# Performance work log

Hardware: AMD Instinct MI355X
Metric: run time of the kernel (lower is better)

The kernel has to match this reference:

```python
import jax, jax.numpy as jnp
import numpy as np

N, D, H = 4096, 256, 8
NEG = -4294967295.0  # -2**32 + 1, as in masked_fill


def _layernorm(x, g, b, eps=1e-5):
    mu = jnp.mean(x, axis=-1, keepdims=True)
    var = jnp.var(x, axis=-1, keepdims=True)
    return (x - mu) * jax.lax.rsqrt(var + eps) * g + b


def setup_inputs() -> dict:
    key = jax.random.key(0)
    ks = jax.random.split(key, 12)
    s = 0.02
    return {
        "x": jax.random.normal(ks[0], (N, D), jnp.float32),
        "mask_idx": jax.random.randint(ks[1], (N,), 0, 2, jnp.int32),
        "spatial": jax.random.normal(ks[2], (N, N), jnp.float32),
        "edge": jax.random.normal(ks[3], (N, N), jnp.float32),
        "ln1_g": jnp.ones((D,), jnp.float32),
        "ln1_b": jnp.zeros((D,), jnp.float32),
        "Wq": jax.random.normal(ks[4], (H, D, D), jnp.float32) * s,
        "bq": jnp.zeros((H, D), jnp.float32),
        "Wk": jax.random.normal(ks[5], (H, D, D), jnp.float32) * s,
        "bk": jnp.zeros((H, D), jnp.float32),
        "Wv": jax.random.normal(ks[6], (H, D, D), jnp.float32) * s,
        "bv": jnp.zeros((H, D), jnp.float32),
        "Wo": jax.random.normal(ks[7], (D, H * D), jnp.float32) * s,
        "bo": jnp.zeros((D,), jnp.float32),
        "ln2_g": jnp.ones((D,), jnp.float32),
        "ln2_b": jnp.zeros((D,), jnp.float32),
        "Wff": jax.random.normal(ks[8], (D, D), jnp.float32) * s,
        "bff": jnp.zeros((D,), jnp.float32),
    }


def reference(x, mask_idx, spatial, edge, ln1_g, ln1_b, Wq, bq, Wk, bk, Wv, bv,
              Wo, bo, ln2_g, ln2_b, Wff, bff):
    x_ln = _layernorm(x, ln1_g, ln1_b)
    # per-head projections, torch Linear: y = x W^T + b ; q,k,v: [H, N, D]
    q = jnp.einsum('nd,hed->hne', x_ln, Wq) + bq[:, None, :]
    k = jnp.einsum('nd,hed->hne', x_ln, Wk) + bk[:, None, :]
    v = jnp.einsum('nd,hed->hne', x_ln, Wv) + bv[:, None, :]
    scale = 1.0 / jnp.sqrt(jnp.float32(D))  # dim_q ** 0.5
    a = jnp.einsum('hne,hme->hnm', q, k) * scale  # [H, N, N]
    a = a + spatial[None] + edge[None]
    mask0 = (mask_idx[:, None] * mask_idx[None, :]) == 0  # [N, N]
    a = jnp.where(mask0[None], jnp.float32(NEG), a)
    p = jax.nn.softmax(a, axis=-1)
    p = jnp.where(mask0[None], 0.0, p)
    heads = jnp.einsum('hnm,hme->hne', p, v)  # [H, N, D]
    cat = jnp.transpose(heads, (1, 0, 2)).reshape(N, H * D)
    x_out = cat @ Wo.T + bo + x
    x_attn = _layernorm(x_out, ln2_g, ln2_b) @ Wff.T + bff + x_out
    return x_attn
```

## Files before the change

### kernel.cpp

```cpp
#include <hip/hip_runtime.h>
#include <hip/hip_bf16.h>
#include <hip/hip_fp16.h>
#include <string.h>

typedef unsigned short u16;
typedef __attribute__((ext_vector_type(8))) short short8;
typedef __attribute__((ext_vector_type(4))) float floatx4;
typedef __attribute__((ext_vector_type(16))) float floatx16;

#define N_TOK 4096
#define D_DIM 256
#define H_HEAD 8

__device__ __forceinline__ u16 f2b(float f){
  __hip_bfloat16 h = __float2bfloat16(f);
  return *reinterpret_cast<u16*>(&h);
}
__device__ __forceinline__ float b2f(u16 u){
  union { unsigned u; float f; } c; c.u = ((unsigned)u) << 16; return c.f;
}
__device__ __forceinline__ float h2f(u16 u){
  __half h; *reinterpret_cast<u16*>(&h) = u; return __half2float(h);
}
__device__ __forceinline__ u16 f2h(float f){
  __half h = __float2half(f); return *reinterpret_cast<u16*>(&h);
}

__device__ __forceinline__ void glds16(const void* g, void* l){
  __builtin_amdgcn_global_load_lds(
      (const __attribute__((address_space(1))) unsigned int*)g,
      (__attribute__((address_space(3))) unsigned int*)l, 16, 0, 0);
}

__global__ void fused_prep(const float* __restrict__ Wq, const float* __restrict__ Wk,
                           const float* __restrict__ Wv, const float* __restrict__ Wo,
                           const float* __restrict__ Wff,
                           const float* __restrict__ bq, const float* __restrict__ bk,
                           const float* __restrict__ bv,
                           u16* __restrict__ wqkv, u16* __restrict__ wo_b,
                           u16* __restrict__ wff_b, float* __restrict__ bqkv){
  int bid = blockIdx.x;
  if (bid == 1056){
    int t = threadIdx.x;
    for (int j = 0; j < 24; ++j){
      int idx = t + j*256;
      float v;
      if (idx < 2048) v = bq[idx];
      else if (idx < 4096) v = bk[idx - 2048];
      else v = bv[idx - 4096];
      bqkv[idx] = v;
    }
    return;
  }
  const float* src; u16* dst; int base;
  if      (bid < 256) { src = Wq;  dst = wqkv;            base = bid; }
  else if (bid < 512) { src = Wk;  dst = wqkv + 524288;   base = bid - 256; }
  else if (bid < 768) { src = Wv;  dst = wqkv + 1048576;  base = bid - 512; }
  else if (bid < 1024){ src = Wo;  dst = wo_b;            base = bid - 768; }
  else                { src = Wff; dst = wff_b;           base = bid - 1024; }
  int i = (base*256 + threadIdx.x)*8;
  float4 a = *(const float4*)(src + i);
  float4 b = *(const float4*)(src + i + 4);
  u16 u[8] = {f2b(a.x),f2b(a.y),f2b(a.z),f2b(a.w),f2b(b.x),f2b(b.y),f2b(b.z),f2b(b.w)};
  *(short8*)(dst + i) = *(short8*)u;
}

__global__ void ln_kernel(const float* __restrict__ x, const float* __restrict__ g,
                          const float* __restrict__ b, u16* __restrict__ out){
  const int row = blockIdx.x;
  const int t = threadIdx.x;
  float v = x[(size_t)row*D_DIM + t];
  float s = v, ss = v*v;
  #pragma unroll
  for (int off = 32; off > 0; off >>= 1){
    s  += __shfl_down(s,  off);
    ss += __shfl_down(ss, off);
  }
  __shared__ float ls[4], lss[4];
  const int w = t >> 6, lane = t & 63;
  if (lane == 0){ ls[w] = s; lss[w] = ss; }
  __syncthreads();
  if (t == 0){
    float S  = ls[0]+ls[1]+ls[2]+ls[3];
    float SS = lss[0]+lss[1]+lss[2]+lss[3];
    float mu = S * (1.0f/D_DIM);
    float var = SS * (1.0f/D_DIM) - mu*mu;
    ls[0] = mu; lss[0] = rsqrtf(var + 1e-5f);
  }
  __syncthreads();
  float mu = ls[0], rs = lss[0];
  out[(size_t)row*D_DIM + t] = f2b((v - mu)*rs*g[t] + b[t]);
}

__global__ void make_biasW(const float* __restrict__ sp, const float* __restrict__ ed,
                           const int* __restrict__ mask, u16* __restrict__ out){
  __shared__ u16 bh[32][64];
  const int tg = blockIdx.x, q32 = blockIdx.y;
  const int t = threadIdx.x;
  const float L2E = 1.4426950408889634f;
  {
    int ql = t>>3, kc = (t&7)*8;
    size_t off = (size_t)(q32*32 + ql)*N_TOK + tg*64 + kc;
    float4 s0 = *(const float4*)(sp + off);
    float4 s1 = *(const float4*)(sp + off + 4);
    float4 e0 = *(const float4*)(ed + off);
    float4 e1 = *(const float4*)(ed + off + 4);
    int mr = mask[q32*32 + ql];
    int4 m0 = *(const int4*)(mask + tg*64 + kc);
    int4 m1 = *(const int4*)(mask + tg*64 + kc + 4);
    bh[ql][kc+0] = f2h((mr*m0.x)==0 ? -60000.f : (s0.x+e0.x)*L2E);
    bh[ql][kc+1] = f2h((mr*m0.y)==0 ? -60000.f : (s0.y+e0.y)*L2E);
    bh[ql][kc+2] = f2h((mr*m0.z)==0 ? -60000.f : (s0.z+e0.z)*L2E);
    bh[ql][kc+3] = f2h((mr*m0.w)==0 ? -60000.f : (s0.w+e0.w)*L2E);
    bh[ql][kc+4] = f2h((mr*m1.x)==0 ? -60000.f : (s1.x+e1.x)*L2E);
    bh[ql][kc+5] = f2h((mr*m1.y)==0 ? -60000.f : (s1.y+e1.y)*L2E);
    bh[ql][kc+6] = f2h((mr*m1.z)==0 ? -60000.f : (s1.z+e1.z)*L2E);
    bh[ql][kc+7] = f2h((mr*m1.w)==0 ? -60000.f : (s1.w+e1.w)*L2E);
  }
  __syncthreads();
  int lane2 = t>>2, j0 = (t&3)*8;
  u16 tmp[8];
  #pragma unroll
  for (int jj = 0; jj < 8; ++jj){
    int j = j0 + jj;
    int nb = j>>4, reg = j&15;
    int kvl = nb*32 + (reg&3) + 8*(reg>>2) + 4*(lane2>>5);
    tmp[jj] = bh[lane2&31][kvl];
  }
  u16* dst = out + (((size_t)q32*64 + tg)*64 + lane2)*32 + j0;
  *(short8*)dst = *(short8*)tmp;
}

__global__ void transpose_v(const u16* __restrict__ v, u16* __restrict__ vt){
  __shared__ u16 t[64][72];
  const int h = blockIdx.z;
  const int n0 = blockIdx.x*64, e0 = blockIdx.y*64;
  const int tid = threadIdx.x;
  const int r = tid >> 2;
  const int c = (tid & 3)*16;
  const u16* src = v + ((size_t)h*N_TOK + n0 + r)*D_DIM + e0 + c;
  short8 a = *(const short8*)src;
  short8 b = *(const short8*)(src + 8);
  #pragma unroll
  for (int i = 0; i < 8; ++i){ t[r][c+i] = ((u16*)&a)[i]; t[r][c+8+i] = ((u16*)&b)[i]; }
  __syncthreads();
  u16 tmp[16];
  #pragma unroll
  for (int i = 0; i < 16; ++i) tmp[i] = t[c+i][r];
  u16* dst = vt + ((size_t)h*D_DIM + e0 + r)*N_TOK + n0 + c;
  *(short8*)dst       = *(short8*)tmp;
  *(short8*)(dst + 8) = *(short8*)(tmp + 8);
}

template<int BM, int BN, int MODE>
__launch_bounds__(256, 2)
__global__ void gemm_bt(const u16* __restrict__ A, const u16* __restrict__ B, int K,
                        const float* __restrict__ bias, const float* __restrict__ resid,
                        void* __restrict__ Cout){
  constexpr int BK = 32;
  constexpr int WM = BM/2, WN = BN/2, FM = WM/16, FN = WN/16;
  constexpr int CApW = BM/64;
  constexpr int CBpW = BN/64;
  __shared__ u16 As[BM*BK];
  __shared__ u16 Bs[BN*BK];
  const int tid = threadIdx.x, w = tid>>6, lane = tid&63;
  const int quad = lane>>4, c16 = lane&15;
  const int wr = w>>1, wc = w&1;
  const int rowT = blockIdx.y*BM, colT = blockIdx.x*BN;
  const int lr = lane>>2;
  const int spos = lane&3;

  floatx4 acc[FM][FN] = {};

  for (int k0 = 0; k0 < K; k0 += BK){
    #pragma unroll
    for (int i = 0; i < CApW; ++i){
      int ch = w*CApW + i;
      int row = ch*16 + lr;
      int gch = spos ^ ((row>>1)&3);
      const u16* g = A + (size_t)(rowT + row)*K + k0 + gch*8;
      glds16(g, As + ch*512);
    }
    #pragma unroll
    for (int i = 0; i < CBpW; ++i){
      int ch = w*CBpW + i;
      int row = ch*16 + lr;
      int gch = spos ^ ((row>>1)&3);
      const u16* g = B + (size_t)(colT + row)*K + k0 + gch*8;
      glds16(g, Bs + ch*512);
    }
    __syncthreads();
    short8 af[FM], bf[FN];
    #pragma unroll
    for (int i = 0; i < FM; ++i){
      int row = wr*WM + i*16 + c16;
      int slot = quad ^ ((row>>1)&3);
      af[i] = *(const short8*)&As[row*BK + slot*8];
    }
    #pragma unroll
    for (int j = 0; j < FN; ++j){
      int row = wc*WN + j*16 + c16;
      int slot = quad ^ ((row>>1)&3);
      bf[j] = *(const short8*)&Bs[row*BK + slot*8];
    }
    #pragma unroll
    for (int i = 0; i < FM; ++i)
      #pragma unroll
      for (int j = 0; j < FN; ++j)
        acc[i][j] = __builtin_amdgcn_mfma_f32_16x16x32_bf16(af[i], bf[j], acc[i][j], 0, 0, 0);
    __syncthreads();
  }

  if (MODE == 0){
    u16* o = (u16*)Cout;
    #pragma unroll
    for (int i = 0; i < FM; ++i)
      #pragma unroll
      for (int j = 0; j < FN; ++j){
        int col = colT + wc*WN + j*16 + c16;
        float bv = bias[col];
        float sc = (col < 2048) ? 0.09016994374947424f : 1.0f;
        size_t obase = (size_t)(col>>8)*((size_t)N_TOK*D_DIM) + (col & 255);
        #pragma unroll
        for (int r = 0; r < 4; ++r){
          int row = rowT + wr*WM + i*16 + quad*4 + r;
          o[obase + (size_t)row*D_DIM] = f2b((acc[i][j][r] + bv)*sc);
        }
      }
  } else {
    float* o = (float*)Cout;
    #pragma unroll
    for (int i = 0; i < FM; ++i)
      #pragma unroll
      for (int j = 0; j < FN; ++j){
        int col = colT + wc*WN + j*16 + c16;
        float bv = bias[col];
        #pragma unroll
        for (int r = 0; r < 4; ++r){
          int row = rowT + wr*WM + i*16 + quad*4 + r;
          size_t idx = (size_t)row*D_DIM + col;
          o[idx] = acc[i][j][r] + bv + resid[idx];
        }
      }
  }
}

__launch_bounds__(512, 2)
__global__ void attn_kernel(const u16* __restrict__ Q, const u16* __restrict__ Kg,
                            const u16* __restrict__ Vt, const u16* __restrict__ biasW,
                            u16* __restrict__ otp0, u16* __restrict__ otp1,
                            float* __restrict__ lsum4){
  extern __shared__ __align__(16) u16 lds[];
  u16* Ks = lds;
  u16* Vs = lds + 16384;
  u16* Ps = lds + 32768;
  const int bx = blockIdx.x, h = blockIdx.y, spl = blockIdx.z;
  const int tid = threadIdx.x, w = tid>>6, lane = tid&63;
  const int hi = lane>>5, l31 = lane&31;
  const int qg = w>>1, kvh = w&1;
  const int eh = w>>1, qh = w&1;
  const int qbase = bx*128;
  const size_t hoff = (size_t)h*N_TOK*D_DIM;
  u16* otp = spl ? otp1 : otp0;

  short8 qf[16];
  {
    const u16* qp = Q + hoff + (size_t)(qbase + qg*32 + l31)*D_DIM + hi*8;
    #pragma unroll
    for (int ks = 0; ks < 16; ++ks) qf[ks] = *(const short8*)(qp + ks*16);
  }

  floatx16 o00 = {}, o01 = {}, o10 = {}, o11 = {};
  float l_lane = 0.f;

  const u16* Kb0 = Kg + hoff + (size_t)spl*2048*D_DIM;
  const u16* Vb0 = Vt + hoff + spl*2048;
  const u16* bWb = biasW + ((((size_t)(bx*4 + qg))*64 + spl*32)*64 + lane)*32 + kvh*16;

  const int krow_s = (w*4)*2;
  {
    const u16* Kb = Kb0;
    const u16* Vb = Vb0;
    #pragma unroll
    for (int i = 0; i < 4; ++i){
      int ch = w*4 + i;
      int row = ch*2 + hi;
      int gch = l31 ^ (row&7);
      glds16(Kb + (size_t)row*D_DIM + gch*8, Ks + ch*512);
      int vrow = ch*8 + (lane>>3);
      int vgch = (lane&7) ^ (vrow&7);
      glds16(Vb + (size_t)vrow*N_TOK + vgch*8, Vs + ch*512);
    }
  }
  __syncthreads();

  for (int t = 0; t < 32; ++t){
    const int tn = (t + 1) & 31;

    const u16* bW = bWb + (size_t)t*64*32;
    short8 bv0 = *(const short8*)(bW);
    short8 bv1 = *(const short8*)(bW + 8);

    floatx16 sa = {}, sb = {};
    const int krow = kvh*32 + l31;
    #pragma unroll
    for (int ks = 0; ks < 16; ++ks){
      int slot = (2*ks + hi) ^ (l31&7);
      short8 ka = *(const short8*)&Ks[krow*256 + slot*8];
      if (ks & 1) sb = __builtin_amdgcn_mfma_f32_32x32x16_bf16(ka, qf[ks], sb, 0, 0, 0);
      else        sa = __builtin_amdgcn_mfma_f32_32x32x16_bf16(ka, qf[ks], sa, 0, 0, 0);
    }

    {
      const int q = qg*32 + l31;
      #pragma unroll
      for (int g = 0; g < 4; ++g){
        float p0, p1, p2, p3;
        {
          u16 b0 = (g < 2) ? ((u16*)&bv0)[4*g+0] : ((u16*)&bv1)[4*(g-2)+0];
          u16 b1 = (g < 2) ? ((u16*)&bv0)[4*g+1] : ((u16*)&bv1)[4*(g-2)+1];
          u16 b2 = (g < 2) ? ((u16*)&bv0)[4*g+2] : ((u16*)&bv1)[4*(g-2)+2];
          u16 b3 = (g < 2) ? ((u16*)&bv0)[4*g+3] : ((u16*)&bv1)[4*(g-2)+3];
          p0 = exp2f(sa[4*g+0] + sb[4*g+0] + h2f(b0) - 23.083120654223414f);
          p1 = exp2f(sa[4*g+1] + sb[4*g+1] + h2f(b1) - 23.083120654223414f);
          p2 = exp2f(sa[4*g+2] + sb[4*g+2] + h2f(b2) - 23.083120654223414f);
          p3 = exp2f(sa[4*g+3] + sb[4*g+3] + h2f(b3) - 23.083120654223414f);
        }
        l_lane += (p0 + p1) + (p2 + p3);
        uint2 pw;
        pw.x = (unsigned)f2b(p0) | ((unsigned)f2b(p1) << 16);
        pw.y = (unsigned)f2b(p2) | ((unsigned)f2b(p3) << 16);
        int slot = (kvh*4 + g) ^ (l31&7);
        *(uint2*)&Ps[q*64 + slot*8 + hi*4] = pw;
      }
    }
    __syncthreads();

    {
      const u16* Kb = Kb0 + (size_t)tn*64*D_DIM;
      #pragma unroll
      for (int i = 0; i < 4; ++i){
        int ch = w*4 + i;
        int row = ch*2 + hi;
        int gch = l31 ^ (row&7);
        glds16(Kb + (size_t)row*D_DIM + gch*8, Ks + ch*512);
      }
    }

    #pragma unroll
    for (int ks2 = 0; ks2 < 4; ++ks2){
      int cA = ks2*2 + hi;
      int slA = cA ^ (l31&7);
      short8 vf0 = *(const short8*)&Vs[(eh*64 +      l31)*64 + slA*8];
      short8 vf1 = *(const short8*)&Vs[(eh*64 + 32 + l31)*64 + slA*8];
      short8 pf0 = *(const short8*)&Ps[(qh*64 +      l31)*64 + slA*8];
      short8 pf1 = *(const short8*)&Ps[(qh*64 + 32 + l31)*64 + slA*8];
      o00 = __builtin_amdgcn_mfma_f32_32x32x16_bf16(vf0, pf0, o00, 0, 0, 0);
      o01 = __builtin_amdgcn_mfma_f32_32x32x16_bf16(vf0, pf1, o01, 0, 0, 0);
      o10 = __builtin_amdgcn_mfma_f32_32x32x16_bf16(vf1, pf0, o10, 0, 0, 0);
      o11 = __builtin_amdgcn_mfma_f32_32x32x16_bf16(vf1, pf1, o11, 0, 0, 0);
    }
    __syncthreads();

    {
      const u16* Vb = Vb0 + tn*64;
      #pragma unroll
      for (int i = 0; i < 4; ++i){
        int ch = w*4 + i;
        int vrow = ch*8 + (lane>>3);
        int vgch = (lane&7) ^ (vrow&7);
        glds16(Vb + (size_t)vrow*N_TOK + vgch*8, Vs + ch*512);
      }
    }
  }

  l_lane += __shfl_xor(l_lane, 32, 64);
  if (hi == 0)
    lsum4[(((size_t)spl*2 + kvh)*H_HEAD + h)*N_TOK + qbase + qg*32 + l31] = l_lane;

  u16* ob = otp + (size_t)h*D_DIM*N_TOK;
  const int qA = qbase + qh*64 + l31;
  #pragma unroll
  for (int reg = 0; reg < 16; ++reg){
    int er = (reg&3) + 8*(reg>>2) + 4*hi;
    int e0 = eh*64 + er;
    ob[(size_t)e0*N_TOK + qA]            = f2b(o00[reg]);
    ob[(size_t)e0*N_TOK + qA + 32]       = f2b(o01[reg]);
    ob[(size_t)(e0+32)*N_TOK + qA]       = f2b(o10[reg]);
    ob[(size_t)(e0+32)*N_TOK + qA + 32]  = f2b(o11[reg]);
  }
}

__global__ void combine_kernel(const u16* __restrict__ o0, const u16* __restrict__ o1,
                               const float* __restrict__ lsum4, u16* __restrict__ cat){
  __shared__ float tile[64][65];
  const int qt = blockIdx.x, et = blockIdx.y, h = blockIdx.z;
  const int t = threadIdx.x;
  {
    int er = t>>2, qc = (t&3)*16;
    size_t base = ((size_t)h*D_DIM + et*64 + er)*N_TOK + qt*64 + qc;
    short8 a0 = *(const short8*)(o0 + base);
    short8 a1 = *(const short8*)(o0 + base + 8);
    short8 b0 = *(const short8*)(o1 + base);
    short8 b1 = *(const short8*)(o1 + base + 8);
    #pragma unroll
    for (int i = 0; i < 8; ++i){
      tile[er][qc+i]   = b2f(((u16*)&a0)[i]) + b2f(((u16*)&b0)[i]);
      tile[er][qc+8+i] = b2f(((u16*)&a1)[i]) + b2f(((u16*)&b1)[i]);
    }
  }
  __syncthreads();
  int qr = t>>2, ec = (t&3)*16;
  int q = qt*64 + qr;
  float l = 0.f;
  #pragma unroll
  for (int s2 = 0; s2 < 4; ++s2)
    l += lsum4[((size_t)s2*H_HEAD + h)*N_TOK + q];
  float inv = (l > 0.f) ? 1.0f/l : 0.f;
  u16 tmp[16];
  #pragma unroll
  for (int i = 0; i < 16; ++i) tmp[i] = f2b(tile[ec+i][qr]*inv);
  u16* cp = cat + (size_t)q*(H_HEAD*D_DIM) + h*D_DIM + et*64 + ec;
  *(short8*)cp     = *(short8*)tmp;
  *(short8*)(cp+8) = *(short8*)(tmp+8);
}

extern "C" void kernel_launch(void* const* d_in, const int* in_sizes, int n_in,
                              void* d_out, int out_size, void* d_ws, size_t ws_size,
                              hipStream_t stream){
  const float* x    = (const float*)d_in[0];
  const int*   mask = (const int*)  d_in[1];
  const float* sp   = (const float*)d_in[2];
  const float* ed   = (const float*)d_in[3];
  const float* g1   = (const float*)d_in[4];
  const float* b1   = (const float*)d_in[5];
  const float* Wq   = (const float*)d_in[6];
  const float* bq   = (const float*)d_in[7];
  const float* Wk   = (const float*)d_in[8];
  const float* bk   = (const float*)d_in[9];
  const float* Wv   = (const float*)d_in[10];
  const float* bv   = (const float*)d_in[11];
  const float* Wo   = (const float*)d_in[12];
  const float* bo   = (const float*)d_in[13];
  const float* g2   = (const float*)d_in[14];
  const float* b2   = (const float*)d_in[15];
  const float* Wff  = (const float*)d_in[16];
  const float* bff  = (const float*)d_in[17];
  float* out = (float*)d_out;
  char* ws = (char*)d_ws;

  constexpr size_t MB = 1ull<<20;
  u16*   wqkv   = (u16*)  (ws + 0);
  u16*   wo_b   = (u16*)  (ws + 3*MB);
  u16*   wff_b  = (u16*)  (ws + 4*MB);
  float* bqkv   = (float*)(ws + 4*MB + 256*1024);
  u16*   xln    = (u16*)  (ws + 4*MB + 512*1024);
  float* lsum4  = (float*)(ws + 6*MB + 512*1024);
  u16*   qkv    = (u16*)  (ws + 7*MB);
  u16*   vt     = (u16*)  (ws + 55*MB);
  u16*   biasW  = (u16*)  (ws + 71*MB);
  u16*   otp1   = (u16*)  (ws + 103*MB);
  u16*   otp0   = (u16*)  (ws + 39*MB);
  u16*   cat    = (u16*)  (ws + 7*MB);
  float* xout   = (float*)(ws + 23*MB);
  u16*   xln2   = (u16*)  (ws + 27*MB);
  const size_t TS = (size_t)H_HEAD*N_TOK*D_DIM;

  fused_prep<<<1057, 256, 0, stream>>>(Wq, Wk, Wv, Wo, Wff, bq, bk, bv,
                                       wqkv, wo_b, wff_b, bqkv);
  ln_kernel<<<N_TOK, 256, 0, stream>>>(x, g1, b1, xln);

  gemm_bt<128,128,0><<<dim3(48, 32), 256, 0, stream>>>(xln, wqkv, 256, bqkv, nullptr, qkv);

  transpose_v<<<dim3(64, 4, 8), 256, 0, stream>>>(qkv + 2*TS, vt);

  make_biasW<<<dim3(64, 128), 256, 0, stream>>>(sp, ed, mask, biasW);

  hipFuncSetAttribute((const void*)attn_kernel,
                      hipFuncAttributeMaxDynamicSharedMemorySize, 81920);
  attn_kernel<<<dim3(32, 8, 2), 512, 81920, stream>>>(qkv, qkv + TS, vt, biasW,
                                                      otp0, otp1, lsum4);

  combine_kernel<<<dim3(64, 4, 8), 256, 0, stream>>>(otp0, otp1, lsum4, cat);

  gemm_bt<64,64,1><<<dim3(4, 64), 256, 0, stream>>>(cat, wo_b, 2048, bo, x, xout);

  ln_kernel<<<N_TOK, 256, 0, stream>>>(xout, g2, b2, xln2);

  gemm_bt<64,64,2><<<dim3(4, 64), 256, 0, stream>>>(xln2, wff_b, 256, bff, xout, out);
}
```

Baseline: 428.4 us.

## Write attention output in cat layout, split-K Wo GEMM, fuse residual+LN2

```diff
diff --git a/kernel.cpp b/kernel.cpp
--- a/kernel.cpp
+++ b/kernel.cpp
@@ -24,6 +24,10 @@
 }
 __device__ __forceinline__ u16 f2h(float f){
   __half h = __float2half(f); return *reinterpret_cast<u16*>(&h);
+}
+__device__ __forceinline__ unsigned pk2bf(float a, float b){
+  __hip_bfloat162 h = __float22bfloat162_rn(make_float2(a, b));
+  return *reinterpret_cast<unsigned*>(&h);
 }
 
 __device__ __forceinline__ void glds16(const void* g, void* l){
@@ -92,12 +96,44 @@
   out[(size_t)row*D_DIM + t] = f2b((v - mu)*rs*g[t] + b[t]);
 }
 
+__global__ void ln_sum(const float* __restrict__ p0, const float* __restrict__ p1,
+                       const float* __restrict__ bo, const float* __restrict__ x,
+                       const float* __restrict__ g, const float* __restrict__ b,
+                       float* __restrict__ xout, u16* __restrict__ xln2){
+  const int row = blockIdx.x;
+  const int t = threadIdx.x;
+  const size_t idx = (size_t)row*D_DIM + t;
+  float v = p0[idx] + p1[idx] + bo[t] + x[idx];
+  float s = v, ss = v*v;
+  #pragma unroll
+  for (int off = 32; off > 0; off >>= 1){
+    s  += __shfl_down(s,  off);
+    ss += __shfl_down(ss, off);
+  }
+  __shared__ float ls[4], lss[4];
+  const int w = t >> 6, lane = t & 63;
+  if (lane == 0){ ls[w] = s; lss[w] = ss; }
+  __syncthreads();
+  if (t == 0){
+    float S  = ls[0]+ls[1]+ls[2]+ls[3];
+    float SS = lss[0]+lss[1]+lss[2]+lss[3];
+    float mu = S * (1.0f/D_DIM);
+    float var = SS * (1.0f/D_DIM) - mu*mu;
+    ls[0] = mu; lss[0] = rsqrtf(var + 1e-5f);
+  }
+  __syncthreads();
+  float mu = ls[0], rs = lss[0];
+  xout[idx] = v;
+  xln2[idx] = f2b((v - mu)*rs*g[t] + b[t]);
+}
+
 __global__ void make_biasW(const float* __restrict__ sp, const float* __restrict__ ed,
                            const int* __restrict__ mask, u16* __restrict__ out){
   __shared__ u16 bh[32][64];
   const int tg = blockIdx.x, q32 = blockIdx.y;
   const int t = threadIdx.x;
   const float L2E = 1.4426950408889634f;
+  const u16 NINF = 0xFC00;
   {
     int ql = t>>3, kc = (t&7)*8;
     size_t off = (size_t)(q32*32 + ql)*N_TOK + tg*64 + kc;
@@ -108,14 +144,14 @@
     int mr = mask[q32*32 + ql];
     int4 m0 = *(const int4*)(mask + tg*64 + kc);
     int4 m1 = *(const int4*)(mask + tg*64 + kc + 4);
-    bh[ql][kc+0] = f2h((mr*m0.x)==0 ? -60000.f : (s0.x+e0.x)*L2E);
-    bh[ql][kc+1] = f2h((mr*m0.y)==0 ? -60000.f : (s0.y+e0.y)*L2E);
-    bh[ql][kc+2] = f2h((mr*m0.z)==0 ? -60000.f : (s0.z+e0.z)*L2E);
-    bh[ql][kc+3] = f2h((mr*m0.w)==0 ? -60000.f : (s0.w+e0.w)*L2E);
-    bh[ql][kc+4] = f2h((mr*m1.x)==0 ? -60000.f : (s1.x+e1.x)*L2E);
-    bh[ql][kc+5] = f2h((mr*m1.y)==0 ? -60000.f : (s1.y+e1.y)*L2E);
-    bh[ql][kc+6] = f2h((mr*m1.z)==0 ? -60000.f : (s1.z+e1.z)*L2E);
-    bh[ql][kc+7] = f2h((mr*m1.w)==0 ? -60000.f : (s1.w+e1.w)*L2E);
+    bh[ql][kc+0] = (mr*m0.x)==0 ? NINF : f2h((s0.x+e0.x)*L2E);
+    bh[ql][kc+1] = (mr*m0.y)==0 ? NINF : f2h((s0.y+e0.y)*L2E);
+    bh[ql][kc+2] = (mr*m0.z)==0 ? NINF : f2h((s0.z+e0.z)*L2E);
+    bh[ql][kc+3] = (mr*m0.w)==0 ? NINF : f2h((s0.w+e0.w)*L2E);
+    bh[ql][kc+4] = (mr*m1.x)==0 ? NINF : f2h((s1.x+e1.x)*L2E);
+    bh[ql][kc+5] = (mr*m1.y)==0 ? NINF : f2h((s1.y+e1.y)*L2E);
+    bh[ql][kc+6] = (mr*m1.z)==0 ? NINF : f2h((s1.z+e1.z)*L2E);
+    bh[ql][kc+7] = (mr*m1.w)==0 ? NINF : f2h((s1.w+e1.w)*L2E);
   }
   __syncthreads();
   int lane2 = t>>2, j0 = (t&3)*8;
@@ -155,6 +191,7 @@
 template<int BM, int BN, int MODE>
 __launch_bounds__(256, 2)
 __global__ void gemm_bt(const u16* __restrict__ A, const u16* __restrict__ B, int K,
+                        int lda, int ldb,
                         const float* __restrict__ bias, const float* __restrict__ resid,
                         void* __restrict__ Cout){
   constexpr int BK = 32;
@@ -169,6 +206,7 @@
   const int rowT = blockIdx.y*BM, colT = blockIdx.x*BN;
   const int lr = lane>>2;
   const int spos = lane&3;
+  const int koff = (MODE == 3) ? (int)blockIdx.z*K : 0;
 
   floatx4 acc[FM][FN] = {};
 
@@ -178,7 +216,7 @@
       int ch = w*CApW + i;
       int row = ch*16 + lr;
       int gch = spos ^ ((row>>1)&3);
-      const u16* g = A + (size_t)(rowT + row)*K + k0 + gch*8;
+      const u16* g = A + (size_t)(rowT + row)*lda + koff + k0 + gch*8;
       glds16(g, As + ch*512);
     }
     #pragma unroll
@@ -186,7 +224,7 @@
       int ch = w*CBpW + i;
       int row = ch*16 + lr;
       int gch = spos ^ ((row>>1)&3);
-      const u16* g = B + (size_t)(colT + row)*K + k0 + gch*8;
+      const u16* g = B + (size_t)(colT + row)*ldb + koff + k0 + gch*8;
       glds16(g, Bs + ch*512);
     }
     __syncthreads();
@@ -227,7 +265,7 @@
           o[obase + (size_t)row*D_DIM] = f2b((acc[i][j][r] + bv)*sc);
         }
       }
-  } else {
+  } else if (MODE == 2){
     float* o = (float*)Cout;
     #pragma unroll
     for (int i = 0; i < FM; ++i)
@@ -242,13 +280,26 @@
           o[idx] = acc[i][j][r] + bv + resid[idx];
         }
       }
+  } else {
+    float* o = (float*)Cout + (size_t)blockIdx.z*((size_t)N_TOK*D_DIM);
+    #pragma unroll
+    for (int i = 0; i < FM; ++i)
+      #pragma unroll
+      for (int j = 0; j < FN; ++j){
+        int col = colT + wc*WN + j*16 + c16;
+        #pragma unroll
+        for (int r = 0; r < 4; ++r){
+          int row = rowT + wr*WM + i*16 + quad*4 + r;
+          o[(size_t)row*D_DIM + col] = acc[i][j][r];
+        }
+      }
   }
 }
 
 __launch_bounds__(512, 2)
 __global__ void attn_kernel(const u16* __restrict__ Q, const u16* __restrict__ Kg,
                             const u16* __restrict__ Vt, const u16* __restrict__ biasW,
-                            u16* __restrict__ otp0, u16* __restrict__ otp1,
+                            u16* __restrict__ cat0, u16* __restrict__ cat1,
                             float* __restrict__ lsum4){
   extern __shared__ __align__(16) u16 lds[];
   u16* Ks = lds;
@@ -258,10 +309,10 @@
   const int tid = threadIdx.x, w = tid>>6, lane = tid&63;
   const int hi = lane>>5, l31 = lane&31;
   const int qg = w>>1, kvh = w&1;
-  const int eh = w>>1, qh = w&1;
+  const int qh = w&1, ev = w>>1;
   const int qbase = bx*128;
   const size_t hoff = (size_t)h*N_TOK*D_DIM;
-  u16* otp = spl ? otp1 : otp0;
+  u16* cs = spl ? cat1 : cat0;
 
   short8 qf[16];
   {
@@ -277,29 +328,24 @@
   const u16* Vb0 = Vt + hoff + spl*2048;
   const u16* bWb = biasW + ((((size_t)(bx*4 + qg))*64 + spl*32)*64 + lane)*32 + kvh*16;
 
-  const int krow_s = (w*4)*2;
+  short8 bv0 = *(const short8*)(bWb);
+  short8 bv1 = *(const short8*)(bWb + 8);
   {
-    const u16* Kb = Kb0;
-    const u16* Vb = Vb0;
     #pragma unroll
     for (int i = 0; i < 4; ++i){
       int ch = w*4 + i;
       int row = ch*2 + hi;
       int gch = l31 ^ (row&7);
-      glds16(Kb + (size_t)row*D_DIM + gch*8, Ks + ch*512);
+      glds16(Kb0 + (size_t)row*D_DIM + gch*8, Ks + ch*512);
       int vrow = ch*8 + (lane>>3);
       int vgch = (lane&7) ^ (vrow&7);
-      glds16(Vb + (size_t)vrow*N_TOK + vgch*8, Vs + ch*512);
+      glds16(Vb0 + (size_t)vrow*N_TOK + vgch*8, Vs + ch*512);
     }
   }
   __syncthreads();
 
   for (int t = 0; t < 32; ++t){
     const int tn = (t + 1) & 31;
-
-    const u16* bW = bWb + (size_t)t*64*32;
-    short8 bv0 = *(const short8*)(bW);
-    short8 bv1 = *(const short8*)(bW + 8);
 
     floatx16 sa = {}, sb = {};
     const int krow = kvh*32 + l31;
@@ -315,21 +361,18 @@
       const int q = qg*32 + l31;
       #pragma unroll
       for (int g = 0; g < 4; ++g){
-        float p0, p1, p2, p3;
-        {
-          u16 b0 = (g < 2) ? ((u16*)&bv0)[4*g+0] : ((u16*)&bv1)[4*(g-2)+0];
-          u16 b1 = (g < 2) ? ((u16*)&bv0)[4*g+1] : ((u16*)&bv1)[4*(g-2)+1];
-          u16 b2 = (g < 2) ? ((u16*)&bv0)[4*g+2] : ((u16*)&bv1)[4*(g-2)+2];
-          u16 b3 = (g < 2) ? ((u16*)&bv0)[4*g+3] : ((u16*)&bv1)[4*(g-2)+3];
-          p0 = exp2f(sa[4*g+0] + sb[4*g+0] + h2f(b0) - 23.083120654223414f);
-          p1 = exp2f(sa[4*g+1] + sb[4*g+1] + h2f(b1) - 23.083120654223414f);
-          p2 = exp2f(sa[4*g+2] + sb[4*g+2] + h2f(b2) - 23.083120654223414f);
-          p3 = exp2f(sa[4*g+3] + sb[4*g+3] + h2f(b3) - 23.083120654223414f);
-        }
+        u16 b0 = (g < 2) ? ((u16*)&bv0)[4*g+0] : ((u16*)&bv1)[4*(g-2)+0];
+        u16 b1 = (g < 2) ? ((u16*)&bv0)[4*g+1] : ((u16*)&bv1)[4*(g-2)+1];
+        u16 b2 = (g < 2) ? ((u16*)&bv0)[4*g+2] : ((u16*)&bv1)[4*(g-2)+2];
+        u16 b3 = (g < 2) ? ((u16*)&bv0)[4*g+3] : ((u16*)&bv1)[4*(g-2)+3];
+        float p0 = exp2f(sa[4*g+0] + sb[4*g+0] + h2f(b0));
+        float p1 = exp2f(sa[4*g+1] + sb[4*g+1] + h2f(b1));
+        float p2 = exp2f(sa[4*g+2] + sb[4*g+2] + h2f(b2));
+        float p3 = exp2f(sa[4*g+3] + sb[4*g+3] + h2f(b3));
         l_lane += (p0 + p1) + (p2 + p3);
         uint2 pw;
-        pw.x = (unsigned)f2b(p0) | ((unsigned)f2b(p1) << 16);
-        pw.y = (unsigned)f2b(p2) | ((unsigned)f2b(p3) << 16);
+        pw.x = pk2bf(p0, p1);
+        pw.y = pk2bf(p2, p3);
         int slot = (kvh*4 + g) ^ (l31&7);
         *(uint2*)&Ps[q*64 + slot*8 + hi*4] = pw;
       }
@@ -345,20 +388,23 @@
         int gch = l31 ^ (row&7);
         glds16(Kb + (size_t)row*D_DIM + gch*8, Ks + ch*512);
       }
+      const u16* bW = bWb + (size_t)tn*64*32;
+      bv0 = *(const short8*)(bW);
+      bv1 = *(const short8*)(bW + 8);
     }
 
     #pragma unroll
     for (int ks2 = 0; ks2 < 4; ++ks2){
       int cA = ks2*2 + hi;
-      int slA = cA ^ (l31&7);
-      short8 vf0 = *(const short8*)&Vs[(eh*64 +      l31)*64 + slA*8];
-      short8 vf1 = *(const short8*)&Vs[(eh*64 + 32 + l31)*64 + slA*8];
-      short8 pf0 = *(const short8*)&Ps[(qh*64 +      l31)*64 + slA*8];
-      short8 pf1 = *(const short8*)&Ps[(qh*64 + 32 + l31)*64 + slA*8];
-      o00 = __builtin_amdgcn_mfma_f32_32x32x16_bf16(vf0, pf0, o00, 0, 0, 0);
-      o01 = __builtin_amdgcn_mfma_f32_32x32x16_bf16(vf0, pf1, o01, 0, 0, 0);
-      o10 = __builtin_amdgcn_mfma_f32_32x32x16_bf16(vf1, pf0, o10, 0, 0, 0);
-      o11 = __builtin_amdgcn_mfma_f32_32x32x16_bf16(vf1, pf1, o11, 0, 0, 0);
+      int sl = cA ^ (l31&7);
+      short8 pf0 = *(const short8*)&Ps[(qh*64 +      l31)*64 + sl*8];
+      short8 pf1 = *(const short8*)&Ps[(qh*64 + 32 + l31)*64 + sl*8];
+      short8 vf0 = *(const short8*)&Vs[(ev*64 +      l31)*64 + sl*8];
+      short8 vf1 = *(const short8*)&Vs[(ev*64 + 32 + l31)*64 + sl*8];
+      o00 = __builtin_amdgcn_mfma_f32_32x32x16_bf16(pf0, vf0, o00, 0, 0, 0);
+      o01 = __builtin_amdgcn_mfma_f32_32x32x16_bf16(pf0, vf1, o01, 0, 0, 0);
+      o10 = __builtin_amdgcn_mfma_f32_32x32x16_bf16(pf1, vf0, o10, 0, 0, 0);
+      o11 = __builtin_amdgcn_mfma_f32_32x32x16_bf16(pf1, vf1, o11, 0, 0, 0);
     }
     __syncthreads();
 
@@ -378,51 +424,38 @@
   if (hi == 0)
     lsum4[(((size_t)spl*2 + kvh)*H_HEAD + h)*N_TOK + qbase + qg*32 + l31] = l_lane;
 
-  u16* ob = otp + (size_t)h*D_DIM*N_TOK;
-  const int qA = qbase + qh*64 + l31;
   #pragma unroll
   for (int reg = 0; reg < 16; ++reg){
-    int er = (reg&3) + 8*(reg>>2) + 4*hi;
-    int e0 = eh*64 + er;
-    ob[(size_t)e0*N_TOK + qA]            = f2b(o00[reg]);
-    ob[(size_t)e0*N_TOK + qA + 32]       = f2b(o01[reg]);
-    ob[(size_t)(e0+32)*N_TOK + qA]       = f2b(o10[reg]);
-    ob[(size_t)(e0+32)*N_TOK + qA + 32]  = f2b(o11[reg]);
-  }
-}
-
-__global__ void combine_kernel(const u16* __restrict__ o0, const u16* __restrict__ o1,
-                               const float* __restrict__ lsum4, u16* __restrict__ cat){
-  __shared__ float tile[64][65];
-  const int qt = blockIdx.x, et = blockIdx.y, h = blockIdx.z;
+    int qr = (reg&3) + 8*(reg>>2) + 4*hi;
+    int q0 = qbase + qh*64 + qr;
+    size_t c0 = (size_t)q0*(H_HEAD*D_DIM) + h*D_DIM + ev*64 + l31;
+    size_t c1 = (size_t)(q0+32)*(H_HEAD*D_DIM) + h*D_DIM + ev*64 + l31;
+    cs[c0]      = f2b(o00[reg]);
+    cs[c0 + 32] = f2b(o01[reg]);
+    cs[c1]      = f2b(o10[reg]);
+    cs[c1 + 32] = f2b(o11[reg]);
+  }
+}
+
+__global__ void combine2(const u16* __restrict__ c0, const u16* __restrict__ c1,
+                         const float* __restrict__ lsum4, u16* __restrict__ cat){
+  const int q = blockIdx.x;
   const int t = threadIdx.x;
-  {
-    int er = t>>2, qc = (t&3)*16;
-    size_t base = ((size_t)h*D_DIM + et*64 + er)*N_TOK + qt*64 + qc;
-    short8 a0 = *(const short8*)(o0 + base);
-    short8 a1 = *(const short8*)(o0 + base + 8);
-    short8 b0 = *(const short8*)(o1 + base);
-    short8 b1 = *(const short8*)(o1 + base + 8);
-    #pragma unroll
-    for (int i = 0; i < 8; ++i){
-      tile[er][qc+i]   = b2f(((u16*)&a0)[i]) + b2f(((u16*)&b0)[i]);
-      tile[er][qc+8+i] = b2f(((u16*)&a1)[i]) + b2f(((u16*)&b1)[i]);
-    }
-  }
-  __syncthreads();
-  int qr = t>>2, ec = (t&3)*16;
-  int q = qt*64 + qr;
+  const int col = t*8;
+  const int h = t >> 5;
   float l = 0.f;
   #pragma unroll
-  for (int s2 = 0; s2 < 4; ++s2)
-    l += lsum4[((size_t)s2*H_HEAD + h)*N_TOK + q];
+  for (int s = 0; s < 4; ++s)
+    l += lsum4[((size_t)s*H_HEAD + h)*N_TOK + q];
   float inv = (l > 0.f) ? 1.0f/l : 0.f;
-  u16 tmp[16];
-  #pragma unroll
-  for (int i = 0; i < 16; ++i) tmp[i] = f2b(tile[ec+i][qr]*inv);
-  u16* cp = cat + (size_t)q*(H_HEAD*D_DIM) + h*D_DIM + et*64 + ec;
-  *(short8*)cp     = *(short8*)tmp;
-  *(short8*)(cp+8) = *(short8*)(tmp+8);
+  size_t base = (size_t)q*(H_HEAD*D_DIM) + col;
+  short8 a = *(const short8*)(c0 + base);
+  short8 b = *(const short8*)(c1 + base);
+  u16 o[8];
+  #pragma unroll
+  for (int i = 0; i < 8; ++i)
+    o[i] = f2b((b2f(((u16*)&a)[i]) + b2f(((u16*)&b)[i]))*inv);
+  *(short8*)(cat + base) = *(short8*)o;
 }
 
 extern "C" void kernel_launch(void* const* d_in, const int* in_sizes, int n_in,
@@ -459,18 +492,20 @@
   u16*   qkv    = (u16*)  (ws + 7*MB);
   u16*   vt     = (u16*)  (ws + 55*MB);
   u16*   biasW  = (u16*)  (ws + 71*MB);
-  u16*   otp1   = (u16*)  (ws + 103*MB);
-  u16*   otp0   = (u16*)  (ws + 39*MB);
+  u16*   cat0   = (u16*)  (ws + 39*MB);
+  u16*   cat1   = (u16*)  (ws + 103*MB);
   u16*   cat    = (u16*)  (ws + 7*MB);
-  float* xout   = (float*)(ws + 23*MB);
-  u16*   xln2   = (u16*)  (ws + 27*MB);
+  float* pK     = (float*)(ws + 23*MB);
+  float* xout   = (float*)(ws + 31*MB);
+  u16*   xln2   = (u16*)  (ws + 35*MB);
   const size_t TS = (size_t)H_HEAD*N_TOK*D_DIM;
 
   fused_prep<<<1057, 256, 0, stream>>>(Wq, Wk, Wv, Wo, Wff, bq, bk, bv,
                                        wqkv, wo_b, wff_b, bqkv);
   ln_kernel<<<N_TOK, 256, 0, stream>>>(x, g1, b1, xln);
 
-  gemm_bt<128,128,0><<<dim3(48, 32), 256, 0, stream>>>(xln, wqkv, 256, bqkv, nullptr, qkv);
+  gemm_bt<128,128,0><<<dim3(48, 32), 256, 0, stream>>>(xln, wqkv, 256, 256, 256,
+                                                       bqkv, nullptr, qkv);
 
   transpose_v<<<dim3(64, 4, 8), 256, 0, stream>>>(qkv + 2*TS, vt);
 
@@ -479,13 +514,16 @@
   hipFuncSetAttribute((const void*)attn_kernel,
                       hipFuncAttributeMaxDynamicSharedMemorySize, 81920);
   attn_kernel<<<dim3(32, 8, 2), 512, 81920, stream>>>(qkv, qkv + TS, vt, biasW,
-                                                      otp0, otp1, lsum4);
-
-  combine_kernel<<<dim3(64, 4, 8), 256, 0, stream>>>(otp0, otp1, lsum4, cat);
-
-  gemm_bt<64,64,1><<<dim3(4, 64), 256, 0, stream>>>(cat, wo_b, 2048, bo, x, xout);
-
-  ln_kernel<<<N_TOK, 256, 0, stream>>>(xout, g2, b2, xln2);
-
-  gemm_bt<64,64,2><<<dim3(4, 64), 256, 0, stream>>>(xln2, wff_b, 256, bff, xout, out);
-}
+                                                      cat0, cat1, lsum4);
+
+  combine2<<<N_TOK, 256, 0, stream>>>(cat0, cat1, lsum4, cat);
+
+  gemm_bt<64,64,3><<<dim3(4, 64, 2), 256, 0, stream>>>(cat, wo_b, 1024, 2048, 2048,
+                                                       nullptr, nullptr, pK);
+
+  ln_sum<<<N_TOK, 256, 0, stream>>>(pK, pK + (size_t)N_TOK*D_DIM, bo, x, g2, b2,
+                                    xout, xln2);
+
+  gemm_bt<64,64,2><<<dim3(4, 64), 256, 0, stream>>>(xln2, wff_b, 256, 256, 256,
+                                                    bff, xout, out);
+}
```

Measured after the change: 422.6 us. Within noise of the previous version (-1.4%).
